# Performance work log

Measured on AMD Instinct MI355X. Metric: run time of the kernel, lower is better.

Reference implementation:

```python
import jax, jax.numpy as jnp
import numpy as np

B, T, N, F, C, H, O = 4, 8, 4096, 32, 32, 64, 1
RADIUS = 50.0   # adjacency_threshold on pairwise distance
EPS = 1e-5      # batchnorm eps


def setup_inputs() -> dict:
    key = jax.random.key(0)
    ks = jax.random.split(key, 8)
    x = jax.random.normal(ks[0], (B, T, N, F), jnp.float32)
    # dist_mat from random 2D node locations in a 1000x1000 area; avg degree ~32
    loc = jax.random.uniform(ks[1], (N, 2), jnp.float32) * 1000.0
    d2 = jnp.sum((loc[:, None, :] - loc[None, :, :]) ** 2, axis=-1)  # [N,N]
    adj = (d2 < RADIUS ** 2).astype(jnp.float32)                     # includes self (d=0)
    dinv = 1.0 / jnp.sqrt(jnp.maximum(adj.sum(-1), 1.0))
    adj_norm = adj * dinv[:, None] * dinv[None, :]                   # D^-1/2 A D^-1/2
    s = 0.05
    return dict(
        x=x,
        adj_norm=adj_norm,
        bn_gamma=jnp.ones((F,), jnp.float32),
        bn_beta=jnp.zeros((F,), jnp.float32),
        W_gcn=jax.random.normal(ks[2], (F, C), jnp.float32) * s,
        b_gcn=jnp.zeros((C,), jnp.float32),
        W_ih=jax.random.normal(ks[3], (C, 3 * H), jnp.float32) * s,
        W_hh=jax.random.normal(ks[4], (H, 3 * H), jnp.float32) * s,
        b_ih=jnp.zeros((3 * H,), jnp.float32),
        b_hh=jnp.zeros((3 * H,), jnp.float32),
        W_dense=jax.random.normal(ks[5], (H, O), jnp.float32) * s,
        b_dense=jnp.zeros((O,), jnp.float32),
    )


def reference(x, adj_norm, bn_gamma, bn_beta, W_gcn, b_gcn, W_ih, W_hh, b_ih, b_hh, W_dense, b_dense):
    # BatchNorm2d over feature channel (training-mode batch stats, biased var)
    mean = x.mean(axis=(0, 1, 2))
    var = x.var(axis=(0, 1, 2))
    xn = (x - mean) * jax.lax.rsqrt(var + EPS) * bn_gamma + bn_beta  # [B,T,N,F]
    # GCN association (same math every timestep -> batch over T)
    ya = jnp.einsum('mn,btnf->btmf', adj_norm, xn)                   # neighbor aggregate
    y = jnp.einsum('btnf,fc->btnc', ya, W_gcn) + b_gcn               # [B,T,N,C]
    # precompute input-gate projections, then scan GRU cell over time
    gi = jnp.einsum('btnc,ch->btnh', y, W_ih) + b_ih                 # [B,T,N,3H]
    gi = jnp.transpose(gi, (1, 0, 2, 3))                             # [T,B,N,3H]

    def step(h, g):
        gh = h @ W_hh + b_hh
        r = jax.nn.sigmoid(g[..., :H] + gh[..., :H])
        z = jax.nn.sigmoid(g[..., H:2 * H] + gh[..., H:2 * H])
        n = jnp.tanh(g[..., 2 * H:] + r * gh[..., 2 * H:])
        h_new = (1.0 - z) * n + z * h
        return h_new, h_new

    h0 = jnp.zeros((B, N, H), x.dtype)
    _, hs = jax.lax.scan(step, h0, gi)                               # [T,B,N,H]
    out = jnp.transpose(hs, (1, 0, 2, 3)) @ W_dense + b_dense        # [B,T,N,O]
    return out
```

## Files before the change

### kernel.cpp

```cpp
#include <hip/hip_runtime.h>
#include <hip/hip_bf16.h>
#include <stdint.h>

#define B_ 4
#define T_ 8
#define N_ 4096
#define F_ 32
#define BT_ (B_*T_)
#define ROWS_ (B_*N_)
#define CAP_ 128
#define EPS_ 1e-5f
#define NELEM_ (B_*T_*N_*F_)

#define WS_BNP    0
#define WS_ROWSUM 16384
#define WS_DEG    (WS_ROWSUM + 4096)
#define WS_FRG    (WS_DEG + 4096)
#define WS_PAIR   (WS_FRG + 52*256)
#define WS_XA     (WS_PAIR + 4096*CAP_*2)
#define WS_X16    (WS_XA + NELEM_)

typedef float v4f __attribute__((ext_vector_type(4)));
typedef _Float16 half8 __attribute__((ext_vector_type(8)));
union HU { uint32_t u[4]; half8 v; };

__device__ inline float sigm_f(float x) {
  return __builtin_amdgcn_rcpf(1.0f + __expf(-x));
}
__device__ inline uint32_t f16pair(float a, float b) {
  union { _Float16 h; unsigned short s; } x, y;
  x.h = (_Float16)a; y.h = (_Float16)b;
  return (uint32_t)x.s | ((uint32_t)y.s << 16);
}
__device__ inline void sp2(float a0, float a1, uint32_t& hi, uint32_t& lo) {
  _Float16 h0 = (_Float16)a0, h1 = (_Float16)a1;
  float r0 = a0 - (float)h0, r1 = a1 - (float)h1;
  union { _Float16 h; unsigned short s; } u0, u1, v0, v1;
  u0.h = h0; u1.h = h1; v0.h = (_Float16)r0; v1.h = (_Float16)r1;
  hi = (uint32_t)u0.s | ((uint32_t)u1.s << 16);
  lo = (uint32_t)v0.s | ((uint32_t)v1.s << 16);
}

__global__ void __launch_bounds__(256)
k_pre(const float* __restrict__ x, const float* __restrict__ A, float* __restrict__ ws) {
  if (blockIdx.x < 2048) {
    int m0 = blockIdx.x * 2;
    __shared__ int cnt[2];
    __shared__ float wsum[4][2];
    if (threadIdx.x < 2) cnt[threadIdx.x] = 0;
    __syncthreads();
    int* deg = (int*)&ws[WS_DEG];
    float2* pair = (float2*)&ws[WS_PAIR];
    const float4* A4 = (const float4*)(A + (size_t)m0 * N_);
    float4 av4[8];
#pragma unroll
    for (int r = 0; r < 2; r++)
#pragma unroll
      for (int i = 0; i < 4; i++) av4[r * 4 + i] = A4[r * 1024 + threadIdx.x + 256 * i];
    float lsum[2] = {0.f, 0.f};
#pragma unroll
    for (int r = 0; r < 2; r++)
#pragma unroll
      for (int i = 0; i < 4; i++) {
        float av[4] = {av4[r*4+i].x, av4[r*4+i].y, av4[r*4+i].z, av4[r*4+i].w};
        int nb4 = (threadIdx.x + 256 * i) * 4;
#pragma unroll
        for (int e = 0; e < 4; e++) {
          float a = av[e];
          if (a != 0.0f) {
            int p = atomicAdd(&cnt[r], 1);
            if (p < CAP_) pair[(size_t)(m0 + r) * CAP_ + p] = make_float2(__int_as_float((nb4 + e) * F_), a);
            lsum[r] += a;
          }
        }
      }
#pragma unroll
    for (int r = 0; r < 2; r++) {
      float s = lsum[r];
#pragma unroll
      for (int off = 32; off > 0; off >>= 1) s += __shfl_xor(s, off, 64);
      if ((threadIdx.x & 63) == 0) wsum[threadIdx.x >> 6][r] = s;
    }
    __syncthreads();
#pragma unroll
    for (int r = 0; r < 2; r++) {
      int c = cnt[r];
      for (int p = c + threadIdx.x; p < 68; p += 256)
        pair[(size_t)(m0 + r) * CAP_ + p] = make_float2(__int_as_float(0), 0.0f);
    }
    if (threadIdx.x < 2) {
      int r = threadIdx.x;
      deg[m0 + r] = min(cnt[r], CAP_);
      ws[WS_ROWSUM + m0 + r] = wsum[0][r] + wsum[1][r] + wsum[2][r] + wsum[3][r];
    }
  } else {
    int bnb = blockIdx.x - 2048;
    const float4* x4 = (const float4*)x;
    uint2* x16 = (uint2*)(ws + WS_X16);
    int tid = bnb * 256 + threadIdx.x;
    float s[4] = {0,0,0,0}, s2[4] = {0,0,0,0};
    for (int i = tid; i < NELEM_ / 4; i += 256 * 256) {
      float4 v = x4[i];
      s[0] += v.x; s2[0] += v.x * v.x;
      s[1] += v.y; s2[1] += v.y * v.y;
      s[2] += v.z; s2[2] += v.z * v.z;
      s[3] += v.w; s2[3] += v.w * v.w;
      int bt = i >> 15, rem = i & 32767, n = rem >> 3, f4 = rem & 7;
      uint2 hp;
      hp.x = f16pair(v.x, v.y);
      hp.y = f16pair(v.z, v.w);
      x16[(size_t)(n * 32 + bt) * 8 + f4] = hp;
    }
    __shared__ float ls[256][4], ls2[256][4];
#pragma unroll
    for (int r = 0; r < 4; r++) { ls[threadIdx.x][r] = s[r]; ls2[threadIdx.x][r] = s2[r]; }
    __syncthreads();
    int t = threadIdx.x;
    if (t < 32) {
      int g = t >> 2, r = t & 3;
      float a = 0.f;
      for (int q = g; q < 256; q += 8) a += ls[q][r];
      ws[WS_BNP + bnb * 64 + t] = a;
    } else if (t < 64) {
      int cch = t - 32;
      int g = cch >> 2, r = cch & 3;
      float b2 = 0.f;
      for (int q = g; q < 256; q += 8) b2 += ls2[q][r];
      ws[WS_BNP + bnb * 64 + t] = b2;
    }
  }
}

#define AGG_STEP(d) { \
    float vv = pv[d]; \
    half8 t0 = pb0[d], t1 = pb1[d]; \
    float2 p = pl[wid * 69 + k + 4 + d]; \
    int nb = __float_as_int(p.x) << 5; \
    pv[d] = p.y; \
    pb0[d] = *(const half8*)(xT + nb + lo0); \
    pb1[d] = *(const half8*)(xT + nb + lo1); \
    _Pragma("unroll") \
    for (int j = 0; j < 8; j++) { \
      acc0[j] += vv * (float)t0[j]; \
      acc1[j] += vv * (float)t1[j]; } }

__global__ void __launch_bounds__(256, 4)
k_aggf(const float* __restrict__ x, const float* __restrict__ gamma,
       const float* __restrict__ beta, const float* __restrict__ Wg,
       const float* __restrict__ bg, const float* __restrict__ Wih,
       const float* __restrict__ bih, const float* __restrict__ Whh,
       const float* __restrict__ bhh, float* __restrict__ ws) {
  __shared__ float2 pl[32 * 69];
  int tid = threadIdx.x;
  if (blockIdx.x >= 1024) {
    float* fs   = (float*)pl;
    float* bnp4 = fs;
    float* bns  = fs + 256;
    float* scl  = fs + 320;
    float* shf  = fs + 352;
    float* ps   = fs + 384;
    float* Wg_s = fs + 416;
    float* Wic  = fs + 1440;
    float* Wxc  = fs + 1952;
    float* UsV  = fs + 2464;
    float* Whc  = fs + 2496;
    int fi = blockIdx.x - 1024;
    int mt, kt;
    if (fi < 32)      { mt = fi >> 2;              kt = fi & 3; }
    else if (fi < 40) { mt = 8 + ((fi - 32) >> 1); kt = (fi & 1) ? 3 : 0; }
    else              { int r = fi - 40; mt = 12 + r / 3; kt = 1 + r % 3; }
    int cls = mt >> 2;
    int colbase = (cls < 2) ? mt * 16 : 128 + (mt & 3) * 16;
    if (kt == 1 || kt == 2) {
      for (int e = tid; e < 512; e += 256) {
        int r = e >> 4, cc = e & 15;
        Whc[e] = Whh[(size_t)((kt - 1) * 32 + r) * 192 + colbase + cc];
      }
    } else {
      ((float4*)Wg_s)[tid] = ((const float4*)Wg)[tid];
      for (int e = tid; e < 512; e += 256) {
        int r = e >> 4, cc = e & 15;
        Wic[e] = Wih[(size_t)r * 192 + colbase + cc];
      }
      int g = tid >> 6, cch = tid & 63;
      float a = 0.f;
      for (int i = 0; i < 64; i++) a += ws[WS_BNP + (size_t)(g + 4 * i) * 64 + cch];
      bnp4[g * 64 + cch] = a;
    }
    __syncthreads();
    if ((kt == 0 || kt == 3) && tid < 64)
      bns[tid] = bnp4[tid] + bnp4[64 + tid] + bnp4[128 + tid] + bnp4[192 + tid];
    __syncthreads();
    if ((kt == 0 || kt == 3) && tid < 32) {
      float cntf = (float)(B_ * T_ * N_);
      float mean = bns[tid] / cntf;
      float var = bns[32 + tid] / cntf - mean * mean;
      float sc = gamma[tid] * rsqrtf(var + EPS_);
      scl[tid] = sc;
      shf[tid] = beta[tid] - mean * sc;
    }
    __syncthreads();
    if (kt == 3 && tid < 32) {
      float acc = 0.f;
#pragma unroll
      for (int f = 0; f < 32; f++) acc += shf[f] * Wg_s[f * 32 + tid];
      ps[tid] = acc;
    }
    __syncthreads();
    if (kt == 0) {
      for (int e = tid; e < 512; e += 256) {
        int f = e >> 4, cc = e & 15;
        float acc = 0.f;
#pragma unroll
        for (int m = 0; m < 32; m++) acc += Wg_s[f * 32 + m] * Wic[m * 16 + cc];
        Wxc[e] = scl[f] * acc;
      }
    } else if (kt == 3) {
      if (tid < 16) {
        float au = 0.f;
#pragma unroll
        for (int c2 = 0; c2 < 32; c2++) au += ps[c2] * Wic[c2 * 16 + tid];
        UsV[tid] = au;
      } else if (tid < 32) {
        int cc = tid - 16;
        float av = 0.f;
#pragma unroll
        for (int c2 = 0; c2 < 32; c2++) av += bg[c2] * Wic[c2 * 16 + cc];
        UsV[16 + cc] = av + bih[colbase + cc];
      }
    }
    __syncthreads();
    if (tid < 64) {
      int L = tid, q = L >> 4, c = L & 15;
      uint32_t* wsu = (uint32_t*)ws;
#pragma unroll
      for (int d = 0; d < 4; d++) {
        float a01[2];
#pragma unroll
        for (int h2 = 0; h2 < 2; h2++) {
          int kk = q * 8 + 2 * d + h2;
          float v;
          if (kt == 0)       v = Wxc[kk * 16 + c];
          else if (kt != 3)  v = Whc[kk * 16 + c];
          else if (kk == 0)  v = (cls == 3) ? 0.f : UsV[c];
          else if (kk == 1)  v = (cls < 2) ? (UsV[16 + c] + bhh[colbase + c])
                                           : (cls == 2 ? UsV[16 + c] : bhh[colbase + c]);
          else               v = 0.f;
          a01[h2] = v;
        }
        wsu[WS_FRG + fi * 256 + L * 4 + d] = f16pair(a01[0], a01[1]);
      }
    }
    return;
  }
  int m0 = blockIdx.x * 4;
  int wid = tid >> 6, L = tid & 63;
  int m = m0 + wid;
  const int* deg = (const int*)&ws[WS_DEG];
  const float2* pair = (const float2*)&ws[WS_PAIR];
  for (int qq = tid; qq < 4 * 68; qq += 256) {
    int r = qq / 68, sl = qq - r * 68;
    pl[r * 69 + sl] = pair[(size_t)(m0 + r) * CAP_ + sl];
  }
  __syncthreads();
  int d0 = deg[m];
  int dm = min(d0, 64);
  int bound = (dm + 3) & ~3;
  const _Float16* xT = (const _Float16*)(ws + WS_X16);
  int lo0 = L * 8, lo1 = 512 + L * 8;
  float acc0[8], acc1[8];
#pragma unroll
  for (int j = 0; j < 8; j++) { acc0[j] = 0.f; acc1[j] = 0.f; }
  half8 pb0[4], pb1[4];
  float pv[4];
#pragma unroll
  for (int d = 0; d < 4; d++) {
    float2 p = pl[wid * 69 + d];
    int nb = __float_as_int(p.x) << 5;
    pv[d] = p.y;
    pb0[d] = *(const half8*)(xT + nb + lo0);
    pb1[d] = *(const half8*)(xT + nb + lo1);
  }
  for (int k = 0; k < bound; k += 4) {
    AGG_STEP(0) AGG_STEP(1) AGG_STEP(2) AGG_STEP(3)
  }
  if (d0 > 64) {
    for (int k = 64; k < d0; k++) {
      float2 p = pair[(size_t)m * CAP_ + k];
      int nb = __float_as_int(p.x) << 5;
      float vv = p.y;
      half8 t0 = *(const half8*)(xT + nb + lo0);
      half8 t1 = *(const half8*)(xT + nb + lo1);
#pragma unroll
      for (int j = 0; j < 8; j++) {
        acc0[j] += vv * (float)t0[j];
        acc1[j] += vv * (float)t1[j];
      }
    }
  }
  int s0 = L >> 2, cg = (L & 3) * 8;
  size_t ob0 = ((size_t)s0 * N_ + m) * F_ + cg;
  size_t ob1 = ((size_t)(s0 + 16) * N_ + m) * F_ + cg;
  v4f w0a = {acc0[0], acc0[1], acc0[2], acc0[3]};
  v4f w0b = {acc0[4], acc0[5], acc0[6], acc0[7]};
  v4f w1a = {acc1[0], acc1[1], acc1[2], acc1[3]};
  v4f w1b = {acc1[4], acc1[5], acc1[6], acc1[7]};
  *(v4f*)(ws + WS_XA + ob0) = w0a;
  *(v4f*)(ws + WS_XA + ob0 + 4) = w0b;
  *(v4f*)(ws + WS_XA + ob1) = w1a;
  *(v4f*)(ws + WS_XA + ob1 + 4) = w1b;
}

#define LDA(fi) (*(const half8*)(frg + (fi)*256 + L*4))
#define DO1(A_, fi, BH, BL) { half8 af = LDA(fi); \
  A_ = __builtin_amdgcn_mfma_f32_16x16x32_f16(af, BH, A_, 0, 0, 0); \
  A_ = __builtin_amdgcn_mfma_f32_16x16x32_f16(af, BL, A_, 0, 0, 0); }
#define DO1C(A_, C_, fi, BH, BL) { half8 af = LDA(fi); \
  A_ = __builtin_amdgcn_mfma_f32_16x16x32_f16(af, BH, C_, 0, 0, 0); \
  A_ = __builtin_amdgcn_mfma_f32_16x16x32_f16(af, BL, A_, 0, 0, 0); }

__global__ void __launch_bounds__(256, 2)
k_gru(const float* __restrict__ Wd, const float* __restrict__ bd,
      const float* __restrict__ ws, float* __restrict__ out) {
  __shared__ uint32_t frg[52 * 256];
  __shared__ uint32_t hx[2 * 1344];
  __shared__ float obuf[2][16];
  {
    const uint4* gf = (const uint4*)(ws + WS_FRG);
    uint4* sf = (uint4*)frg;
    for (int i = threadIdx.x; i < 52 * 64; i += 256) sf[i] = gf[i];
  }
  __syncthreads();
  int wid = threadIdx.x >> 6, L = threadIdx.x & 63;
  int grp = wid >> 1, half = wid & 1, h2 = half * 2;
  int q = L >> 4, c = L & 15;
  uint32_t* hxg = hx + grp * 1344;
  int rg0 = blockIdx.x * 32 + grp * 16;
  int b = rg0 >> 12;
  int node0 = rg0 & (N_ - 1);
  int fR0 = 4 * h2, fR1 = 4 * h2 + 4;
  int fZ0 = 16 + 4 * h2, fZ1 = 20 + 4 * h2;
  int fN0 = 32 + 2 * h2, fN1 = 34 + 2 * h2;
  int fG0 = 40 + 3 * h2, fG1 = 43 + 3 * h2;
  float wdv[2][4];
#pragma unroll
  for (int lg = 0; lg < 2; lg++)
#pragma unroll
    for (int r = 0; r < 4; r++) wdv[lg][r] = Wd[16 * (h2 + lg) + 4 * q + r];
  float bdv = bd[0];

  HU b3h, b3l;
#pragma unroll
  for (int d = 0; d < 4; d++) { b3h.u[d] = 0; b3l.u[d] = 0; }
  {
    float rsv = ws[WS_ROWSUM + node0 + c];
    uint32_t rhi, rlo;
    sp2(rsv, 1.0f, rhi, rlo);
    if (q == 0) { b3h.u[0] = rhi; b3l.u[0] = rlo & 0xFFFFu; }
  }

  v4f bias[8];
  {
    v4f z4 = {0.f, 0.f, 0.f, 0.f};
    DO1C(bias[0], z4, fR0 + 3, b3h.v, b3l.v)
    DO1C(bias[1], z4, fR1 + 3, b3h.v, b3l.v)
    DO1C(bias[2], z4, fZ0 + 3, b3h.v, b3l.v)
    DO1C(bias[3], z4, fZ1 + 3, b3h.v, b3l.v)
    DO1C(bias[4], z4, fN0 + 1, b3h.v, b3l.v)
    DO1C(bias[5], z4, fN1 + 1, b3h.v, b3l.v)
    DO1C(bias[6], z4, fG0 + 2, b3h.v, b3l.v)
    DO1C(bias[7], z4, fG1 + 2, b3h.v, b3l.v)
  }

  float h[2][4];
#pragma unroll
  for (int lg = 0; lg < 2; lg++)
#pragma unroll
    for (int r = 0; r < 4; r++) h[lg][r] = 0.f;

  const float* xab = ws + WS_XA;
  size_t xo0 = ((size_t)(b * T_) * N_ + node0 + c) * F_ + q * 8;
  float4 curA = *(const float4*)(xab + xo0);
  float4 curB = *(const float4*)(xab + xo0 + 4);
  float4 nxA, nxB;

#pragma unroll 1
  for (int t = 0; t < T_; t++) {
    HU b1h, b1l, b2h, b2l;
    if (t > 0) {
#pragma unroll
      for (int d = 0; d < 4; d++) {
        b1h.u[d] = hxg[((4 * q + d) * 2 + 0) * 21 + c];
        b1l.u[d] = hxg[((4 * q + d) * 2 + 1) * 21 + c];
        b2h.u[d] = hxg[((16 + 4 * q + d) * 2 + 0) * 21 + c];
        b2l.u[d] = hxg[((16 + 4 * q + d) * 2 + 1) * 21 + c];
      }
    }
    __syncthreads();
    if (t < T_ - 1) {
      size_t xo = ((size_t)(b * T_ + t + 1) * N_ + node0 + c) * F_ + q * 8;
      nxA = *(const float4*)(xab + xo);
      nxB = *(const float4*)(xab + xo + 4);
    }
    HU b0h, b0l;
    sp2(curA.x, curA.y, b0h.u[0], b0l.u[0]);
    sp2(curA.z, curA.w, b0h.u[1], b0l.u[1]);
    sp2(curB.x, curB.y, b0h.u[2], b0l.u[2]);
    sp2(curB.z, curB.w, b0h.u[3], b0l.u[3]);
    v4f acc[8];
    if (t > 0) {
      DO1C(acc[0], bias[0], fR0 + 1, b1h.v, b1l.v)
      DO1C(acc[1], bias[1], fR1 + 1, b1h.v, b1l.v)
      DO1C(acc[2], bias[2], fZ0 + 1, b1h.v, b1l.v)
      DO1C(acc[3], bias[3], fZ1 + 1, b1h.v, b1l.v)
      DO1C(acc[6], bias[6], fG0,     b1h.v, b1l.v)
      DO1C(acc[7], bias[7], fG1,     b1h.v, b1l.v)
      DO1(acc[0], fR0 + 2, b2h.v, b2l.v)
      DO1(acc[1], fR1 + 2, b2h.v, b2l.v)
      DO1(acc[2], fZ0 + 2, b2h.v, b2l.v)
      DO1(acc[3], fZ1 + 2, b2h.v, b2l.v)
      DO1(acc[6], fG0 + 1, b2h.v, b2l.v)
      DO1(acc[7], fG1 + 1, b2h.v, b2l.v)
      DO1(acc[0], fR0, b0h.v, b0l.v)
      DO1(acc[1], fR1, b0h.v, b0l.v)
      DO1(acc[2], fZ0, b0h.v, b0l.v)
      DO1(acc[3], fZ1, b0h.v, b0l.v)
      DO1C(acc[4], bias[4], fN0, b0h.v, b0l.v)
      DO1C(acc[5], bias[5], fN1, b0h.v, b0l.v)
    } else {
      DO1C(acc[0], bias[0], fR0, b0h.v, b0l.v)
      DO1C(acc[1], bias[1], fR1, b0h.v, b0l.v)
      DO1C(acc[2], bias[2], fZ0, b0h.v, b0l.v)
      DO1C(acc[3], bias[3], fZ1, b0h.v, b0l.v)
      DO1C(acc[4], bias[4], fN0, b0h.v, b0l.v)
      DO1C(acc[5], bias[5], fN1, b0h.v, b0l.v)
      acc[6] = bias[6]; acc[7] = bias[7];
    }
    float o = 0.f;
#pragma unroll
    for (int lg = 0; lg < 2; lg++)
#pragma unroll
      for (int r = 0; r < 4; r++) {
        float rr = sigm_f(acc[lg][r]);
        float zz = sigm_f(acc[2 + lg][r]);
        float nn = 2.0f * sigm_f(2.0f * (acc[4 + lg][r] + rr * acc[6 + lg][r])) - 1.0f;
        float hn = zz * (h[lg][r] - nn) + nn;
        h[lg][r] = hn;
        o += wdv[lg][r] * hn;
      }
    o += __shfl_xor(o, 16, 64);
    o += __shfl_xor(o, 32, 64);
    if (half == 1 && L < 16) obuf[grp][L] = o;
    if (t < T_ - 1) {
#pragma unroll
      for (int lg = 0; lg < 2; lg++)
#pragma unroll
        for (int rp = 0; rp < 2; rp++) {
          uint32_t phi, plo;
          sp2(h[lg][2 * rp], h[lg][2 * rp + 1], phi, plo);
          int pidx = 8 * (h2 + lg) + 2 * q + rp;
          hxg[(pidx * 2 + 0) * 21 + c] = phi;
          hxg[(pidx * 2 + 1) * 21 + c] = plo;
        }
    }
    __syncthreads();
    if (half == 0 && L < 16)
      out[(size_t)(b * T_ + t) * N_ + node0 + L] = o + obuf[grp][L] + bdv;
    curA = nxA; curB = nxB;
  }
}

extern "C" void kernel_launch(void* const* d_in, const int* in_sizes, int n_in,
                              void* d_out, int out_size, void* d_ws, size_t ws_size,
                              hipStream_t stream) {
  const float* x     = (const float*)d_in[0];
  const float* adj   = (const float*)d_in[1];
  const float* gamma = (const float*)d_in[2];
  const float* beta  = (const float*)d_in[3];
  const float* Wg    = (const float*)d_in[4];
  const float* bg    = (const float*)d_in[5];
  const float* Wih   = (const float*)d_in[6];
  const float* Whh   = (const float*)d_in[7];
  const float* bih   = (const float*)d_in[8];
  const float* bhh   = (const float*)d_in[9];
  const float* Wd    = (const float*)d_in[10];
  const float* bd    = (const float*)d_in[11];
  float* ws = (float*)d_ws;
  float* out = (float*)d_out;

  k_pre<<<2048 + 256, 256, 0, stream>>>(x, adj, ws);
  k_aggf<<<1024 + 52, 256, 0, stream>>>(x, gamma, beta, Wg, bg, Wih, bih, Whh, bhh, ws);
  k_gru<<<512, 256, 0, stream>>>(Wd, bd, ws, out);
}
```

Measured before the change: 167.9 us.

## Double-buffer GRU hidden state, prefetch all timesteps, single barrier per step

The GRU kernel now double-buffers the hidden-state exchange in shared memory, so each timestep needs one lightweight barrier (lgkmcnt wait plus s_barrier) instead of two __syncthreads. It loads all eight timesteps of aggregated input into registers up front and fully unrolls the time loop. Output partial sums are buffered and written once after the loop, which removes the per-step cross-wave reduction through shared memory. This raises register and LDS pressure, which may reduce occupancy under launch_bounds(256,2).

```diff
diff --git a/kernel.cpp b/kernel.cpp
--- a/kernel.cpp
+++ b/kernel.cpp
@@ -318,13 +318,16 @@
 #define DO1C(A_, C_, fi, BH, BL) { half8 af = LDA(fi); \
   A_ = __builtin_amdgcn_mfma_f32_16x16x32_f16(af, BH, C_, 0, 0, 0); \
   A_ = __builtin_amdgcn_mfma_f32_16x16x32_f16(af, BL, A_, 0, 0, 0); }
+#define LBAR() { asm volatile("s_waitcnt lgkmcnt(0)" ::: "memory"); \
+  __builtin_amdgcn_s_barrier(); \
+  __builtin_amdgcn_sched_barrier(0); }
 
 __global__ void __launch_bounds__(256, 2)
 k_gru(const float* __restrict__ Wd, const float* __restrict__ bd,
       const float* __restrict__ ws, float* __restrict__ out) {
   __shared__ uint32_t frg[52 * 256];
-  __shared__ uint32_t hx[2 * 1344];
-  __shared__ float obuf[2][16];
+  __shared__ uint32_t hx[2][2][1344];
+  __shared__ float obuf[2][8][16];
   {
     const uint4* gf = (const uint4*)(ws + WS_FRG);
     uint4* sf = (uint4*)frg;
@@ -334,7 +337,6 @@
   int wid = threadIdx.x >> 6, L = threadIdx.x & 63;
   int grp = wid >> 1, half = wid & 1, h2 = half * 2;
   int q = L >> 4, c = L & 15;
-  uint32_t* hxg = hx + grp * 1344;
   int rg0 = blockIdx.x * 32 + grp * 16;
   int b = rg0 >> 12;
   int node0 = rg0 & (N_ - 1);
@@ -348,6 +350,15 @@
 #pragma unroll
     for (int r = 0; r < 4; r++) wdv[lg][r] = Wd[16 * (h2 + lg) + 4 * q + r];
   float bdv = bd[0];
+
+  const float* xab = ws + WS_XA;
+  float4 xaA[T_], xaB[T_];
+#pragma unroll
+  for (int t = 0; t < T_; t++) {
+    size_t xo = ((size_t)(b * T_ + t) * N_ + node0 + c) * F_ + q * 8;
+    xaA[t] = *(const float4*)(xab + xo);
+    xaB[t] = *(const float4*)(xab + xo + 4);
+  }
 
   HU b3h, b3l;
 #pragma unroll
@@ -377,36 +388,26 @@
   for (int lg = 0; lg < 2; lg++)
 #pragma unroll
     for (int r = 0; r < 4; r++) h[lg][r] = 0.f;
-
-  const float* xab = ws + WS_XA;
-  size_t xo0 = ((size_t)(b * T_) * N_ + node0 + c) * F_ + q * 8;
-  float4 curA = *(const float4*)(xab + xo0);
-  float4 curB = *(const float4*)(xab + xo0 + 4);
-  float4 nxA, nxB;
-
-#pragma unroll 1
+  float o8[T_];
+
+#pragma unroll
   for (int t = 0; t < T_; t++) {
     HU b1h, b1l, b2h, b2l;
     if (t > 0) {
+      const uint32_t* hb = hx[grp][(t - 1) & 1];
 #pragma unroll
       for (int d = 0; d < 4; d++) {
-        b1h.u[d] = hxg[((4 * q + d) * 2 + 0) * 21 + c];
-        b1l.u[d] = hxg[((4 * q + d) * 2 + 1) * 21 + c];
-        b2h.u[d] = hxg[((16 + 4 * q + d) * 2 + 0) * 21 + c];
-        b2l.u[d] = hxg[((16 + 4 * q + d) * 2 + 1) * 21 + c];
-      }
-    }
-    __syncthreads();
-    if (t < T_ - 1) {
-      size_t xo = ((size_t)(b * T_ + t + 1) * N_ + node0 + c) * F_ + q * 8;
-      nxA = *(const float4*)(xab + xo);
-      nxB = *(const float4*)(xab + xo + 4);
+        b1h.u[d] = hb[((4 * q + d) * 2 + 0) * 21 + c];
+        b1l.u[d] = hb[((4 * q + d) * 2 + 1) * 21 + c];
+        b2h.u[d] = hb[((16 + 4 * q + d) * 2 + 0) * 21 + c];
+        b2l.u[d] = hb[((16 + 4 * q + d) * 2 + 1) * 21 + c];
+      }
     }
     HU b0h, b0l;
-    sp2(curA.x, curA.y, b0h.u[0], b0l.u[0]);
-    sp2(curA.z, curA.w, b0h.u[1], b0l.u[1]);
-    sp2(curB.x, curB.y, b0h.u[2], b0l.u[2]);
-    sp2(curB.z, curB.w, b0h.u[3], b0l.u[3]);
+    sp2(xaA[t].x, xaA[t].y, b0h.u[0], b0l.u[0]);
+    sp2(xaA[t].z, xaA[t].w, b0h.u[1], b0l.u[1]);
+    sp2(xaB[t].x, xaB[t].y, b0h.u[2], b0l.u[2]);
+    sp2(xaB[t].z, xaB[t].w, b0h.u[3], b0l.u[3]);
     v4f acc[8];
     if (t > 0) {
       DO1C(acc[0], bias[0], fR0 + 1, b1h.v, b1l.v)
@@ -450,8 +451,9 @@
       }
     o += __shfl_xor(o, 16, 64);
     o += __shfl_xor(o, 32, 64);
-    if (half == 1 && L < 16) obuf[grp][L] = o;
+    o8[t] = o;
     if (t < T_ - 1) {
+      uint32_t* hb = hx[grp][t & 1];
 #pragma unroll
       for (int lg = 0; lg < 2; lg++)
 #pragma unroll
@@ -459,14 +461,21 @@
           uint32_t phi, plo;
           sp2(h[lg][2 * rp], h[lg][2 * rp + 1], phi, plo);
           int pidx = 8 * (h2 + lg) + 2 * q + rp;
-          hxg[(pidx * 2 + 0) * 21 + c] = phi;
-          hxg[(pidx * 2 + 1) * 21 + c] = plo;
+          hb[(pidx * 2 + 0) * 21 + c] = phi;
+          hb[(pidx * 2 + 1) * 21 + c] = plo;
         }
-    }
-    __syncthreads();
-    if (half == 0 && L < 16)
-      out[(size_t)(b * T_ + t) * N_ + node0 + L] = o + obuf[grp][L] + bdv;
-    curA = nxA; curB = nxB;
+      LBAR()
+    }
+  }
+  if (half == 1 && L < 16) {
+#pragma unroll
+    for (int t = 0; t < T_; t++) obuf[grp][t][L] = o8[t];
+  }
+  LBAR()
+  if (half == 0 && L < 16) {
+#pragma unroll
+    for (int t = 0; t < T_; t++)
+      out[(size_t)(b * T_ + t) * N_ + node0 + L] = o8[t] + obuf[grp][t][L] + bdv;
   }
 }
 
```

Result: no change. 168.2 us (+0.2%).
